# Kernel tuning notes

Measured on AMD Instinct MI355X. Metric: run time of the kernel, lower is better.

Reference implementation:

```python
import jax, jax.numpy as jnp
import numpy as np

D_MODEL = 2048
N_HEADS = 16
N_KV_HEADS = 4
HEAD_DIM = D_MODEL // N_HEADS  # 128
N_REP = N_HEADS // N_KV_HEADS  # 4
ROPE_BASE = 10000.0


def _rope_tables(T, head_dim, dtype):
    inv_freq = 1.0 / (ROPE_BASE ** (jnp.arange(0, head_dim, 2, dtype=jnp.float32) / head_dim))
    t = jnp.arange(T, dtype=jnp.float32)
    freqs = jnp.outer(t, inv_freq)               # [T, hd/2]
    emb = jnp.concatenate([freqs, freqs], axis=-1)  # [T, hd]
    return jnp.cos(emb).astype(dtype), jnp.sin(emb).astype(dtype)


def _rotate_half(x):
    x1, x2 = jnp.split(x, 2, axis=-1)
    return jnp.concatenate([-x2, x1], axis=-1)


def _apply_rope(x, cos, sin):
    # x: [B, H, T, hd]; cos/sin: [T, hd]
    return x * cos[None, None] + _rotate_half(x) * sin[None, None]


def setup_inputs() -> dict:
    key = jax.random.key(0)
    ks = jax.random.split(key, 5)
    B, T = 2, 2048
    s_in = 1.0 / np.sqrt(D_MODEL)
    return {
        "x": jax.random.normal(ks[0], (B, T, D_MODEL), jnp.float32),
        "Wq": jax.random.normal(ks[1], (D_MODEL, D_MODEL), jnp.float32) * s_in,
        "Wk": jax.random.normal(ks[2], (D_MODEL, N_KV_HEADS * HEAD_DIM), jnp.float32) * s_in,
        "Wv": jax.random.normal(ks[3], (D_MODEL, N_KV_HEADS * HEAD_DIM), jnp.float32) * s_in,
        "Wo": jax.random.normal(ks[4], (D_MODEL, D_MODEL), jnp.float32) * s_in,
    }


def reference(x, Wq, Wk, Wv, Wo):
    B, T, C = x.shape
    scale = HEAD_DIM ** -0.5
    q = (x @ Wq).reshape(B, T, N_HEADS, HEAD_DIM).transpose(0, 2, 1, 3)     # [B,H,T,hd]
    k = (x @ Wk).reshape(B, T, N_KV_HEADS, HEAD_DIM).transpose(0, 2, 1, 3)  # [B,Hkv,T,hd]
    v = (x @ Wv).reshape(B, T, N_KV_HEADS, HEAD_DIM).transpose(0, 2, 1, 3)
    cos, sin = _rope_tables(T, HEAD_DIM, x.dtype)
    q = _apply_rope(q, cos, sin)
    k = _apply_rope(k, cos, sin)
    # GQA: group query heads; avoid materializing expanded K/V
    qg = q.reshape(B, N_KV_HEADS, N_REP, T, HEAD_DIM)
    scores = jnp.einsum('bgrtd,bgsd->bgrts', qg, k) * scale                 # [B,Hkv,rep,T,S]
    causal = jnp.tril(jnp.ones((T, T), dtype=bool))
    scores = jnp.where(causal[None, None, None], scores, jnp.finfo(scores.dtype).min)
    attn = jax.nn.softmax(scores, axis=-1)
    out = jnp.einsum('bgrts,bgsd->bgrtd', attn, v)                          # [B,Hkv,rep,T,hd]
    out = out.reshape(B, N_HEADS, T, HEAD_DIM).transpose(0, 2, 1, 3).reshape(B, T, C)
    return out @ Wo, k, v
```

## Files before the change

### kernel.cpp

```cpp
#include <hip/hip_runtime.h>
#include <hip/hip_bf16.h>
#include <type_traits>


typedef short  short8 __attribute__((ext_vector_type(8)));
typedef float  f32x4  __attribute__((ext_vector_type(4)));
typedef float  f32x16 __attribute__((ext_vector_type(16)));

#define AS1(p) ((__attribute__((address_space(1))) void*)(p))
#define AS3(p) ((__attribute__((address_space(3))) void*)(p))

static __device__ inline short bf_bits(float f) {
    __hip_bfloat16 h = __float2bfloat16(f);
    return *reinterpret_cast<short*>(&h);
}

__global__ __launch_bounds__(256) void convert_x_kernel(
    const float* __restrict__ x, __hip_bfloat16* __restrict__ xb)
{
    int i = (blockIdx.x * 256 + threadIdx.x) * 4;
    float4 v = *reinterpret_cast<const float4*>(x + i);
    ushort4 o;
    o.x = (unsigned short)bf_bits(v.x);
    o.y = (unsigned short)bf_bits(v.y);
    o.z = (unsigned short)bf_bits(v.z);
    o.w = (unsigned short)bf_bits(v.w);
    *reinterpret_cast<ushort4*>(reinterpret_cast<unsigned short*>(xb) + i) = o;
}

__global__ void transpose_convert_kernel(
    const float* __restrict__ W, __hip_bfloat16* __restrict__ WT, int K, int N)
{
    __shared__ float tile[32][33];
    int n0 = blockIdx.x * 32, k0 = blockIdx.y * 32;
    int tx = threadIdx.x, ty = threadIdx.y;
#pragma unroll
    for (int i = 0; i < 32; i += 8)
        tile[ty + i][tx] = W[(size_t)(k0 + ty + i) * N + n0 + tx];
    __syncthreads();
#pragma unroll
    for (int i = 0; i < 32; i += 8)
        WT[(size_t)(n0 + ty + i) * K + k0 + tx] = __float2bfloat16(tile[tx][ty + i]);
}

template <typename CT>
__global__ __launch_bounds__(256) void gemm_bt_kernel(
    const __hip_bfloat16* __restrict__ A,
    const __hip_bfloat16* __restrict__ BT,
    CT* __restrict__ C, int M, int N, int K)
{
    const int tid  = threadIdx.x;
    const int w    = tid >> 6;
    const int lane = tid & 63;
    const int l31  = lane & 31;
    const int hi   = lane >> 5;
    const int m0 = blockIdx.y << 7;
    const int n0 = blockIdx.x << 7;
    const int wm = (w >> 1) << 6;
    const int wn = (w & 1) << 6;

    __shared__ __hip_bfloat16 As[128 * 64];
    __shared__ __hip_bfloat16 Bs[128 * 64];

    f32x16 acc[2][2] = {};

    for (int k0 = 0; k0 < K; k0 += 64) {
#pragma unroll
        for (int i = 0; i < 4; ++i) {
            int c = tid + i * 256;
            int row = c >> 3;
            int soct = (c & 7) ^ (row & 7);
            const __hip_bfloat16* ga = A  + (size_t)(m0 + row) * K + k0 + soct * 8;
            const __hip_bfloat16* gb = BT + (size_t)(n0 + row) * K + k0 + soct * 8;
            __builtin_amdgcn_global_load_lds(AS1(ga), AS3(As + c * 8), 16, 0, 0);
            __builtin_amdgcn_global_load_lds(AS1(gb), AS3(Bs + c * 8), 16, 0, 0);
        }
        __syncthreads();

#pragma unroll
        for (int ks = 0; ks < 4; ++ks) {
            const int oct = ((ks * 2 + hi) ^ (l31 & 7)) << 3;
            short8 a[2], b[2];
#pragma unroll
            for (int mi = 0; mi < 2; ++mi)
                a[mi] = *reinterpret_cast<const short8*>(
                    reinterpret_cast<const short*>(As) + (wm + mi * 32 + l31) * 64 + oct);
#pragma unroll
            for (int ni = 0; ni < 2; ++ni)
                b[ni] = *reinterpret_cast<const short8*>(
                    reinterpret_cast<const short*>(Bs) + (wn + ni * 32 + l31) * 64 + oct);
#pragma unroll
            for (int mi = 0; mi < 2; ++mi)
#pragma unroll
                for (int ni = 0; ni < 2; ++ni)
                    acc[mi][ni] = __builtin_amdgcn_mfma_f32_32x32x16_bf16(
                        a[mi], b[ni], acc[mi][ni], 0, 0, 0);
        }
        __syncthreads();
    }

#pragma unroll
    for (int mi = 0; mi < 2; ++mi)
#pragma unroll
        for (int ni = 0; ni < 2; ++ni)
#pragma unroll
            for (int reg = 0; reg < 16; ++reg) {
                int row = m0 + wm + mi * 32 + (reg & 3) + 8 * (reg >> 2) + 4 * hi;
                int col = n0 + wn + ni * 32 + l31;
                float v = acc[mi][ni][reg];
                if constexpr (std::is_same<CT, float>::value)
                    C[(size_t)row * N + col] = v;
                else
                    C[(size_t)row * N + col] = __float2bfloat16(v);
            }
}

__global__ __launch_bounds__(256) void gemm_qkv_fused(
    const __hip_bfloat16* __restrict__ A,
    const __hip_bfloat16* __restrict__ BT,
    __hip_bfloat16* __restrict__ qkv,
    float* __restrict__ outk,
    float* __restrict__ outv,
    __hip_bfloat16* __restrict__ VT)
{
    const int tid  = threadIdx.x;
    const int w    = tid >> 6;
    const int lane = tid & 63;
    const int l31  = lane & 31;
    const int hi   = lane >> 5;
    const int m0 = blockIdx.y << 7;
    const int n0 = blockIdx.x << 7;
    const int wm = w << 5;
    const int K = 2048;

    __shared__ __hip_bfloat16 As[128 * 64];
    __shared__ __hip_bfloat16 Bs[128 * 64];

    f32x16 acc[4] = {};

    for (int k0 = 0; k0 < K; k0 += 64) {
#pragma unroll
        for (int i = 0; i < 4; ++i) {
            int c = tid + i * 256;
            int row = c >> 3;
            int soct = (c & 7) ^ (row & 7);
            const __hip_bfloat16* ga = A  + (size_t)(m0 + row) * K + k0 + soct * 8;
            const __hip_bfloat16* gb = BT + (size_t)(n0 + row) * K + k0 + soct * 8;
            __builtin_amdgcn_global_load_lds(AS1(ga), AS3(As + c * 8), 16, 0, 0);
            __builtin_amdgcn_global_load_lds(AS1(gb), AS3(Bs + c * 8), 16, 0, 0);
        }
        __syncthreads();

#pragma unroll
        for (int ks = 0; ks < 4; ++ks) {
            const int oct = ((ks * 2 + hi) ^ (l31 & 7)) << 3;
            short8 a = *reinterpret_cast<const short8*>(
                reinterpret_cast<const short*>(As) + (wm + l31) * 64 + oct);
#pragma unroll
            for (int ni = 0; ni < 4; ++ni) {
                short8 b = *reinterpret_cast<const short8*>(
                    reinterpret_cast<const short*>(Bs) + (ni * 32 + l31) * 64 + oct);
                acc[ni] = __builtin_amdgcn_mfma_f32_32x32x16_bf16(a, b, acc[ni], 0, 0, 0);
            }
        }
        __syncthreads();
    }

    const int hc = n0 >> 7;
    if (hc < 20) {
        float invf[2];
#pragma unroll
        for (int ni = 0; ni < 2; ++ni)
            invf[ni] = exp2f((float)(ni * 32 + l31) * -0.20762050593046f);
#pragma unroll
        for (int reg = 0; reg < 16; ++reg) {
            int row = m0 + wm + (reg & 3) + 8 * (reg >> 2) + 4 * hi;
            int b = row >> 11, t = row & 2047;
#pragma unroll
            for (int ni = 0; ni < 2; ++ni) {
                int d = ni * 32 + l31;
                float ang = (float)t * invf[ni];
                float s = __sinf(ang), c = __cosf(ang);
                float x1 = acc[ni][reg], x2 = acc[ni + 2][reg];
                float o1 = x1 * c - x2 * s;
                float o2 = x2 * c + x1 * s;
                __hip_bfloat16* q = qkv + (size_t)row * 3072 + hc * 128 + d;
                q[0]  = __float2bfloat16(o1);
                q[64] = __float2bfloat16(o2);
                if (hc >= 16) {
                    int kh = hc - 16;
                    float* ok = outk + (size_t)((b * 4 + kh) * 2048 + t) * 128 + d;
                    ok[0]  = o1;
                    ok[64] = o2;
                }
            }
        }
    } else {
        const int kh = hc - 20;
#pragma unroll
        for (int reg = 0; reg < 16; ++reg) {
            int row = m0 + wm + (reg & 3) + 8 * (reg >> 2) + 4 * hi;
            int b = row >> 11, t = row & 2047;
#pragma unroll
            for (int ni = 0; ni < 4; ++ni) {
                int d = ni * 32 + l31;
                float v = acc[ni][reg];
                outv[(size_t)((b * 4 + kh) * 2048 + t) * 128 + d] = v;
                VT[(size_t)((b * 4 + kh) * 128 + d) * 2048 + t] = __float2bfloat16(v);
            }
        }
    }
}

__global__ __launch_bounds__(256, 2) void attn_kernel(
    const __hip_bfloat16* __restrict__ qkv,
    const __hip_bfloat16* __restrict__ VT,
    __hip_bfloat16* __restrict__ outO)
{
    const int bh = blockIdx.x;
    const int b = bh >> 4, h = bh & 15;
    const int kh = h >> 2;
    const int yb = blockIdx.y;
    const int qblk = (yb < 8) ? (15 - yb) : (yb - 8);
    const int tid = threadIdx.x;
    const int w = tid >> 6;
    const int lane = tid & 63;
    const int lo16 = lane & 15, grp = lane >> 4;
    const int qrow0 = qblk * 128 + w * 32;

    __shared__ short Ks[2][64 * 128];
    __shared__ short Vs[2][128 * 64];
    __shared__ short Ps[4][32 * 64];

    const short* qkvs = reinterpret_cast<const short*>(qkv);
    const size_t kbase = (size_t)b * 2048 * 3072 + 2048 + kh * 128;
    const short* vtb = reinterpret_cast<const short*>(VT) + (size_t)(b * 4 + kh) * 128 * 2048;
    short* pw = &Ps[w][0];

    short8 qf[2][4];
#pragma unroll
    for (int mi = 0; mi < 2; ++mi) {
        const short* qp = qkvs + (size_t)(b * 2048 + qrow0 + mi * 16 + lo16) * 3072
                        + h * 128 + grp * 8;
#pragma unroll
        for (int ss = 0; ss < 4; ++ss)
            qf[mi][ss] = *reinterpret_cast<const short8*>(qp + ss * 32);
    }

    f32x4 o[2][8] = {};
    f32x4 lac[2] = {};

    short8 ones;
#pragma unroll
    for (int jj = 0; jj < 8; ++jj) ones[jj] = (short)0x3F80;

    const float scl2 = 0.12752749545902973f;
    const int ntiles = qblk * 2 + 2;

#define STAGE(buf, kb_)                                                              \
    {                                                                                \
        _Pragma("unroll")                                                            \
        for (int i = 0; i < 4; ++i) {                                                \
            int c = tid + i * 256;                                                   \
            int row = c >> 4, c16 = (c & 15) ^ (row & 7);                            \
            const short* src = qkvs + kbase + (size_t)((kb_) + row) * 3072 + c16 * 8;\
            __builtin_amdgcn_global_load_lds(AS1(src),                               \
                AS3(&Ks[buf][(w * 64 + i * 256) * 8]), 16, 0, 0);                    \
        }                                                                            \
        _Pragma("unroll")                                                            \
        for (int i = 0; i < 4; ++i) {                                                \
            int c = tid + i * 256;                                                   \
            int d = c >> 3, c8 = (c & 7) ^ (d & 7);                                  \
            const short* src = vtb + (size_t)d * 2048 + (kb_) + c8 * 8;              \
            __builtin_amdgcn_global_load_lds(AS1(src),                               \
                AS3(&Vs[buf][(w * 64 + i * 256) * 8]), 16, 0, 0);                    \
        }                                                                            \
    }

    STAGE(0, 0);
    __syncthreads();
    int cur = 0;

    for (int t = 0; t < ntiles; ++t) {
        const int kb = t * 64;
        if (t + 1 < ntiles) STAGE(cur ^ 1, kb + 64);

        f32x4 sg[2][4];
        __builtin_amdgcn_s_setprio(1);
#pragma unroll
        for (int kg = 0; kg < 4; ++kg) {
            f32x4 a0 = {}, a1 = {};
#pragma unroll
            for (int ss = 0; ss < 4; ++ss) {
                short8 kf = *reinterpret_cast<const short8*>(
                    &Ks[cur][(kg * 16 + lo16) * 128 + (((ss * 4 + grp) ^ (lo16 & 7)) << 3)]);
                a0 = __builtin_amdgcn_mfma_f32_16x16x32_bf16(qf[0][ss], kf, a0, 0, 0, 0);
                a1 = __builtin_amdgcn_mfma_f32_16x16x32_bf16(qf[1][ss], kf, a1, 0, 0, 0);
            }
            sg[0][kg] = a0; sg[1][kg] = a1;
        }
        __builtin_amdgcn_s_setprio(0);

        if (kb + 63 > qrow0) {
#pragma unroll
            for (int mi = 0; mi < 2; ++mi)
#pragma unroll
                for (int kg = 0; kg < 4; ++kg) {
                    const int key = kb + kg * 16 + lo16;
#pragma unroll
                    for (int r = 0; r < 4; ++r) {
                        float v = sg[mi][kg][r] * scl2;
                        sg[mi][kg][r] = (key <= qrow0 + mi * 16 + grp * 4 + r) ? v : -1e30f;
                    }
                }
        } else {
#pragma unroll
            for (int mi = 0; mi < 2; ++mi)
#pragma unroll
                for (int kg = 0; kg < 4; ++kg)
#pragma unroll
                    for (int r = 0; r < 4; ++r) sg[mi][kg][r] *= scl2;
        }

#pragma unroll
        for (int mi = 0; mi < 2; ++mi)
#pragma unroll
            for (int kg = 0; kg < 4; ++kg)
#pragma unroll
                for (int r = 0; r < 4; ++r) {
                    float p = __builtin_amdgcn_exp2f(sg[mi][kg][r]);
                    int row = mi * 16 + grp * 4 + r;
                    int idx = row * 64 + (((kg * 2 + (lo16 >> 3)) ^ (row & 7)) << 3) + (lo16 & 7);
                    pw[idx] = bf_bits(p);
                }

        __builtin_amdgcn_s_setprio(1);
#pragma unroll
        for (int ks = 0; ks < 2; ++ks) {
            short8 pf0 = *reinterpret_cast<const short8*>(
                &pw[(0 * 16 + lo16) * 64 + (((ks * 4 + grp) ^ (lo16 & 7)) << 3)]);
            short8 pf1 = *reinterpret_cast<const short8*>(
                &pw[(1 * 16 + lo16) * 64 + (((ks * 4 + grp) ^ (lo16 & 7)) << 3)]);
            lac[0] = __builtin_amdgcn_mfma_f32_16x16x32_bf16(pf0, ones, lac[0], 0, 0, 0);
            lac[1] = __builtin_amdgcn_mfma_f32_16x16x32_bf16(pf1, ones, lac[1], 0, 0, 0);
#pragma unroll
            for (int jj = 0; jj < 8; ++jj) {
                short8 vf = *reinterpret_cast<const short8*>(
                    &Vs[cur][(jj * 16 + lo16) * 64 + (((ks * 4 + grp) ^ (lo16 & 7)) << 3)]);
                o[0][jj] = __builtin_amdgcn_mfma_f32_16x16x32_bf16(pf0, vf, o[0][jj], 0, 0, 0);
                o[1][jj] = __builtin_amdgcn_mfma_f32_16x16x32_bf16(pf1, vf, o[1][jj], 0, 0, 0);
            }
        }
        __builtin_amdgcn_s_setprio(0);

        __syncthreads();
        cur ^= 1;
    }
#undef STAGE

#pragma unroll
    for (int mi = 0; mi < 2; ++mi)
#pragma unroll
        for (int r = 0; r < 4; ++r) {
            float inv = 1.0f / lac[mi][r];
#pragma unroll
            for (int jj = 0; jj < 8; ++jj) {
                outO[(size_t)(b * 2048 + qrow0 + mi * 16 + grp * 4 + r) * 2048
                     + h * 128 + jj * 16 + lo16] = __float2bfloat16(o[mi][jj][r] * inv);
            }
        }
}

extern "C" void kernel_launch(void* const* d_in, const int* in_sizes, int n_in,
                              void* d_out, int out_size, void* d_ws, size_t ws_size,
                              hipStream_t stream)
{
    (void)in_sizes; (void)n_in; (void)out_size; (void)ws_size;
    const float* x  = (const float*)d_in[0];
    const float* Wq = (const float*)d_in[1];
    const float* Wk = (const float*)d_in[2];
    const float* Wv = (const float*)d_in[3];
    const float* Wo = (const float*)d_in[4];

    float* out0 = (float*)d_out;
    float* outk = out0 + 8388608;
    float* outv = out0 + 10485760;

    __hip_bfloat16* wsb    = (__hip_bfloat16*)d_ws;
    __hip_bfloat16* xb     = wsb;
    __hip_bfloat16* WqkvT  = xb + 8388608;
    __hip_bfloat16* WoT    = WqkvT + 6291456;
    __hip_bfloat16* qkv    = WoT + 4194304;
    __hip_bfloat16* VT     = qkv + 12582912;
    __hip_bfloat16* attn_o = xb;

    convert_x_kernel<<<8192, 256, 0, stream>>>(x, xb);
    transpose_convert_kernel<<<dim3(64, 64), dim3(32, 8), 0, stream>>>(Wq, WqkvT, 2048, 2048);
    transpose_convert_kernel<<<dim3(16, 64), dim3(32, 8), 0, stream>>>(Wk, WqkvT + (size_t)2048 * 2048, 2048, 512);
    transpose_convert_kernel<<<dim3(16, 64), dim3(32, 8), 0, stream>>>(Wv, WqkvT + (size_t)2560 * 2048, 2048, 512);
    transpose_convert_kernel<<<dim3(64, 64), dim3(32, 8), 0, stream>>>(Wo, WoT, 2048, 2048);

    gemm_qkv_fused<<<dim3(24, 32), 256, 0, stream>>>(xb, WqkvT, qkv, outk, outv, VT);

    attn_kernel<<<dim3(32, 16), 256, 0, stream>>>(qkv, VT, attn_o);

    gemm_bt_kernel<float><<<dim3(16, 32), 256, 0, stream>>>(attn_o, WoT, out0, 4096, 2048, 2048);
}
```

Measured before the change: 204.9 us.

## Double-buffer GEMM LDS tiles and remap blocks per XCD for L2 locality

Both GEMM kernels now use two LDS buffers. The next K-slice is issued with global_load_lds while MFMAs run on the current slice, removing the load-then-sync stall at each iteration. The launch grid is also flattened to 1D, and a decode groups M-tiles by XCD (bid & 7) so blocks sharing A rows land on the same L2. Double buffering doubles LDS use to 64KB per block, which may reduce occupancy. The loop also keeps one __syncthreads per iteration, and whether the prefetch overlaps depends on how the async loads are waited on.

```diff
diff --git a/kernel.cpp b/kernel.cpp
--- a/kernel.cpp
+++ b/kernel.cpp
@@ -43,6 +43,18 @@
         WT[(size_t)(n0 + ty + i) * K + k0 + tx] = __float2bfloat16(tile[tx][ty + i]);
 }
 
+static __device__ inline void xcd_decode(int bid, int M, int N, int& m0, int& n0)
+{
+    const int xcd = bid & 7;
+    const int idx = bid >> 3;
+    const int mpx = (M >> 7) >> 3;
+    const int rem = idx % (mpx * 4);
+    const int mb = xcd * mpx + rem % mpx;
+    const int nb = (idx / (mpx * 4)) * 4 + rem / mpx;
+    m0 = mb << 7;
+    n0 = nb << 7;
+}
+
 template <typename CT>
 __global__ __launch_bounds__(256) void gemm_bt_kernel(
     const __hip_bfloat16* __restrict__ A,
@@ -54,28 +66,37 @@
     const int lane = tid & 63;
     const int l31  = lane & 31;
     const int hi   = lane >> 5;
-    const int m0 = blockIdx.y << 7;
-    const int n0 = blockIdx.x << 7;
+    int m0, n0;
+    xcd_decode(blockIdx.x, M, N, m0, n0);
     const int wm = (w >> 1) << 6;
     const int wn = (w & 1) << 6;
 
-    __shared__ __hip_bfloat16 As[128 * 64];
-    __shared__ __hip_bfloat16 Bs[128 * 64];
+    __shared__ __hip_bfloat16 As[2][128 * 64];
+    __shared__ __hip_bfloat16 Bs[2][128 * 64];
 
     f32x16 acc[2][2] = {};
 
-    for (int k0 = 0; k0 < K; k0 += 64) {
-#pragma unroll
-        for (int i = 0; i < 4; ++i) {
-            int c = tid + i * 256;
-            int row = c >> 3;
-            int soct = (c & 7) ^ (row & 7);
-            const __hip_bfloat16* ga = A  + (size_t)(m0 + row) * K + k0 + soct * 8;
-            const __hip_bfloat16* gb = BT + (size_t)(n0 + row) * K + k0 + soct * 8;
-            __builtin_amdgcn_global_load_lds(AS1(ga), AS3(As + c * 8), 16, 0, 0);
-            __builtin_amdgcn_global_load_lds(AS1(gb), AS3(Bs + c * 8), 16, 0, 0);
-        }
-        __syncthreads();
+#define GSTAGE(buf, k0_)                                                            \
+    {                                                                               \
+        _Pragma("unroll")                                                           \
+        for (int i = 0; i < 4; ++i) {                                               \
+            int c = tid + i * 256;                                                  \
+            int row = c >> 3;                                                       \
+            int soct = (c & 7) ^ (row & 7);                                         \
+            const __hip_bfloat16* ga = A  + (size_t)(m0 + row) * K + (k0_) + soct * 8; \
+            const __hip_bfloat16* gb = BT + (size_t)(n0 + row) * K + (k0_) + soct * 8; \
+            __builtin_amdgcn_global_load_lds(AS1(ga), AS3(&As[buf][c * 8]), 16, 0, 0); \
+            __builtin_amdgcn_global_load_lds(AS1(gb), AS3(&Bs[buf][c * 8]), 16, 0, 0); \
+        }                                                                           \
+    }
+
+    GSTAGE(0, 0);
+    __syncthreads();
+    int cur = 0;
+    const int nk = K >> 6;
+
+    for (int t = 0; t < nk; ++t) {
+        if (t + 1 < nk) GSTAGE(cur ^ 1, (t + 1) << 6);
 
 #pragma unroll
         for (int ks = 0; ks < 4; ++ks) {
@@ -84,11 +105,11 @@
 #pragma unroll
             for (int mi = 0; mi < 2; ++mi)
                 a[mi] = *reinterpret_cast<const short8*>(
-                    reinterpret_cast<const short*>(As) + (wm + mi * 32 + l31) * 64 + oct);
+                    reinterpret_cast<const short*>(&As[cur][0]) + (wm + mi * 32 + l31) * 64 + oct);
 #pragma unroll
             for (int ni = 0; ni < 2; ++ni)
                 b[ni] = *reinterpret_cast<const short8*>(
-                    reinterpret_cast<const short*>(Bs) + (wn + ni * 32 + l31) * 64 + oct);
+                    reinterpret_cast<const short*>(&Bs[cur][0]) + (wn + ni * 32 + l31) * 64 + oct);
 #pragma unroll
             for (int mi = 0; mi < 2; ++mi)
 #pragma unroll
@@ -97,7 +118,9 @@
                         a[mi], b[ni], acc[mi][ni], 0, 0, 0);
         }
         __syncthreads();
-    }
+        cur ^= 1;
+    }
+#undef GSTAGE
 
 #pragma unroll
     for (int mi = 0; mi < 2; ++mi)
@@ -128,43 +151,53 @@
     const int lane = tid & 63;
     const int l31  = lane & 31;
     const int hi   = lane >> 5;
-    const int m0 = blockIdx.y << 7;
-    const int n0 = blockIdx.x << 7;
+    int m0, n0;
+    xcd_decode(blockIdx.x, 4096, 3072, m0, n0);
     const int wm = w << 5;
     const int K = 2048;
 
-    __shared__ __hip_bfloat16 As[128 * 64];
-    __shared__ __hip_bfloat16 Bs[128 * 64];
+    __shared__ __hip_bfloat16 As[2][128 * 64];
+    __shared__ __hip_bfloat16 Bs[2][128 * 64];
 
     f32x16 acc[4] = {};
 
-    for (int k0 = 0; k0 < K; k0 += 64) {
-#pragma unroll
-        for (int i = 0; i < 4; ++i) {
-            int c = tid + i * 256;
-            int row = c >> 3;
-            int soct = (c & 7) ^ (row & 7);
-            const __hip_bfloat16* ga = A  + (size_t)(m0 + row) * K + k0 + soct * 8;
-            const __hip_bfloat16* gb = BT + (size_t)(n0 + row) * K + k0 + soct * 8;
-            __builtin_amdgcn_global_load_lds(AS1(ga), AS3(As + c * 8), 16, 0, 0);
-            __builtin_amdgcn_global_load_lds(AS1(gb), AS3(Bs + c * 8), 16, 0, 0);
-        }
-        __syncthreads();
+#define GSTAGE(buf, k0_)                                                            \
+    {                                                                               \
+        _Pragma("unroll")                                                           \
+        for (int i = 0; i < 4; ++i) {                                               \
+            int c = tid + i * 256;                                                  \
+            int row = c >> 3;                                                       \
+            int soct = (c & 7) ^ (row & 7);                                         \
+            const __hip_bfloat16* ga = A  + (size_t)(m0 + row) * K + (k0_) + soct * 8; \
+            const __hip_bfloat16* gb = BT + (size_t)(n0 + row) * K + (k0_) + soct * 8; \
+            __builtin_amdgcn_global_load_lds(AS1(ga), AS3(&As[buf][c * 8]), 16, 0, 0); \
+            __builtin_amdgcn_global_load_lds(AS1(gb), AS3(&Bs[buf][c * 8]), 16, 0, 0); \
+        }                                                                           \
+    }
+
+    GSTAGE(0, 0);
+    __syncthreads();
+    int cur = 0;
+
+    for (int t = 0; t < 32; ++t) {
+        if (t + 1 < 32) GSTAGE(cur ^ 1, (t + 1) << 6);
 
 #pragma unroll
         for (int ks = 0; ks < 4; ++ks) {
             const int oct = ((ks * 2 + hi) ^ (l31 & 7)) << 3;
             short8 a = *reinterpret_cast<const short8*>(
-                reinterpret_cast<const short*>(As) + (wm + l31) * 64 + oct);
+                reinterpret_cast<const short*>(&As[cur][0]) + (wm + l31) * 64 + oct);
 #pragma unroll
             for (int ni = 0; ni < 4; ++ni) {
                 short8 b = *reinterpret_cast<const short8*>(
-                    reinterpret_cast<const short*>(Bs) + (ni * 32 + l31) * 64 + oct);
+                    reinterpret_cast<const short*>(&Bs[cur][0]) + (ni * 32 + l31) * 64 + oct);
                 acc[ni] = __builtin_amdgcn_mfma_f32_32x32x16_bf16(a, b, acc[ni], 0, 0, 0);
             }
         }
         __syncthreads();
-    }
+        cur ^= 1;
+    }
+#undef GSTAGE
 
     const int hc = n0 >> 7;
     if (hc < 20) {
@@ -400,9 +433,9 @@
     transpose_convert_kernel<<<dim3(16, 64), dim3(32, 8), 0, stream>>>(Wv, WqkvT + (size_t)2560 * 2048, 2048, 512);
     transpose_convert_kernel<<<dim3(64, 64), dim3(32, 8), 0, stream>>>(Wo, WoT, 2048, 2048);
 
-    gemm_qkv_fused<<<dim3(24, 32), 256, 0, stream>>>(xb, WqkvT, qkv, outk, outv, VT);
+    gemm_qkv_fused<<<768, 256, 0, stream>>>(xb, WqkvT, qkv, outk, outv, VT);
 
     attn_kernel<<<dim3(32, 16), 256, 0, stream>>>(qkv, VT, attn_o);
 
-    gemm_bt_kernel<float><<<dim3(16, 32), 256, 0, stream>>>(attn_o, WoT, out0, 4096, 2048, 2048);
-}
+    gemm_bt_kernel<float><<<512, 256, 0, stream>>>(attn_o, WoT, out0, 4096, 2048, 2048);
+}
```

Result: no change. 203.2 us (-0.8%).
